# Optimization experiments

Measured on AMD Instinct MI355X. Metric: run time of the kernel, lower is better.

## Reference

```python
import jax, jax.numpy as jnp
import numpy as np

N, E, D, H, L = 50000, 400000, 128, 256, 2
ZR = 0.8          # z_ratio
GN_EPS = 1e-5     # PyG GraphNorm eps


def _graph_norm(x, w, b, a):
    # PyG GraphNorm on a single graph: x - mean_scale*mean, rms-normalize
    mu = jnp.mean(x, axis=0, keepdims=True)
    xc = x - a * mu
    var = jnp.mean(xc * xc, axis=0, keepdims=True)
    return w * xc / jnp.sqrt(var + GN_EPS) + b


def _gat(x, src, dst, W, a_src, a_dst, bias):
    # PyG GATConv, heads=1, add_self_loops=True, negative_slope=0.2.
    # edge_dim is None -> edge_attr is ignored by the layer.
    n = x.shape[0]
    loop = jnp.arange(n)
    s = jnp.concatenate([src, loop])   # [E+N]
    d = jnp.concatenate([dst, loop])
    xw = x @ W.T                        # [N,H]
    logit = jax.nn.leaky_relu((xw @ a_src)[s] + (xw @ a_dst)[d], 0.2)
    m = jax.ops.segment_max(logit, d, num_segments=n)
    ex = jnp.exp(logit - m[d])
    den = jax.ops.segment_sum(ex, d, num_segments=n)
    alpha = ex / (den[d] + 1e-16)
    return jax.ops.segment_sum(alpha[:, None] * xw[s], d, num_segments=n) + bias


def _mix(x0, x1, mask):
    return jnp.where(mask, ZR * x1 + (1.0 - ZR) * x0, ZR * x0 + (1.0 - ZR) * x1)


def _forward(x_, edge_index, edge_attr, question_embeddings, subgraph_mask,
             node_in_W, node_in_b, edge_in_W, edge_in_b, q_in_W, q_in_b,
             nqm_W, nqm_b, eqm_W, eqm_b,
             t0_W, t0_b, t1_W, t1_b,
             gat_W, gat_asrc, gat_adst, gat_bias,
             cgn_w, cgn_b, cgn_a,
             c0_W, c0_b, c1_W, c1_b,
             gn_w, gn_b, gn_a, final_W, final_b):
    src, dst = edge_index[0], edge_index[1]
    mask = subgraph_mask[:, None]
    x = jax.nn.relu(x_ @ node_in_W.T + node_in_b)                 # [N,H]
    e = jax.nn.relu(edge_attr @ edge_in_W.T + edge_in_b)          # [E,H] (unused by GAT: lin_edge is None)
    q = jax.nn.relu(question_embeddings @ q_in_W.T + q_in_b)[0]   # [1,H]
    n = x.shape[0]
    for l in range(L):
        qx = jnp.broadcast_to(q, (n, H))
        xc = jax.nn.relu(jnp.concatenate([x, qx], axis=-1) @ nqm_W[l].T + nqm_b[l])
        # torch also computes e_combined = relu(edge_question_mix([e,q])) but GATConv
        # (edge_dim=None) ignores it, so it is dead code: omitted.
        x1 = jax.nn.relu(xc @ t1_W[l].T + t1_b[l])
        x0 = jax.nn.relu(xc @ t0_W[l].T + t0_b[l])
        h = _mix(x0, x1, mask)
        h = _gat(h, src, dst, gat_W[l], gat_asrc[l], gat_adst[l], gat_bias[l])
        h = _graph_norm(h, cgn_w[l], cgn_b[l], cgn_a[l])
        # dropout p=0 -> no-op
        hc = jnp.concatenate([h, xc], axis=-1)                    # [N,2H]
        x1 = hc @ c1_W[l].T + c1_b[l]
        x0 = hc @ c0_W[l].T + c0_b[l]
        x = _mix(x0, x1, mask)
        x = _graph_norm(x, gn_w[l], gn_b[l], gn_a[l])
    # masked mean/max/add pooling over subgraph nodes (single graph)
    mk = mask.astype(x.dtype)
    cnt = jnp.sum(mk)
    x_add = jnp.sum(x * mk, axis=0, keepdims=True)
    x_mean = x_add / jnp.maximum(cnt, 1.0)
    x_max = jnp.max(jnp.where(mask, x, -jnp.inf), axis=0, keepdims=True)
    pooled = jnp.concatenate([x_mean, x_max, x_add], axis=-1)     # [1,3H]
    return pooled @ final_W.T + final_b                           # [1,H]


def setup_inputs() -> dict:
    keys = jax.random.split(jax.random.key(0), 64)
    it = iter(range(64))
    def nx(shape, s=0.05):
        return jax.random.normal(keys[next(it)], shape, jnp.float32) * s
    inp = {}
    inp['x_'] = jax.random.normal(keys[next(it)], (N, D), jnp.float32)
    inp['edge_index'] = jax.random.randint(keys[next(it)], (2, E), 0, N)
    inp['edge_attr'] = jax.random.normal(keys[next(it)], (E, D), jnp.float32)
    inp['question_embeddings'] = jax.random.normal(keys[next(it)], (1, 1, D), jnp.float32)
    inp['subgraph_mask'] = jax.random.bernoulli(keys[next(it)], 0.5, (N,))
    inp['node_in_W'] = nx((H, D)); inp['node_in_b'] = nx((H,))
    inp['edge_in_W'] = nx((H, D)); inp['edge_in_b'] = nx((H,))
    inp['q_in_W'] = nx((H, D));    inp['q_in_b'] = nx((H,))
    inp['nqm_W'] = nx((L, H, 2 * H)); inp['nqm_b'] = nx((L, H))
    inp['eqm_W'] = nx((L, H, 2 * H)); inp['eqm_b'] = nx((L, H))
    inp['t0_W'] = nx((L, H, H)); inp['t0_b'] = nx((L, H))
    inp['t1_W'] = nx((L, H, H)); inp['t1_b'] = nx((L, H))
    inp['gat_W'] = nx((L, H, H)); inp['gat_asrc'] = nx((L, H))
    inp['gat_adst'] = nx((L, H)); inp['gat_bias'] = nx((L, H))
    inp['cgn_w'] = jnp.ones((L, H)); inp['cgn_b'] = jnp.zeros((L, H)); inp['cgn_a'] = jnp.ones((L, H))
    inp['c0_W'] = nx((L, H, 2 * H)); inp['c0_b'] = nx((L, H))
    inp['c1_W'] = nx((L, H, 2 * H)); inp['c1_b'] = nx((L, H))
    inp['gn_w'] = jnp.ones((L, H)); inp['gn_b'] = jnp.zeros((L, H)); inp['gn_a'] = jnp.ones((L, H))
    inp['final_W'] = nx((H, 3 * H)); inp['final_b'] = nx((H,))
    return inp


def reference(x_, edge_index, edge_attr, question_embeddings, subgraph_mask,
              node_in_W, node_in_b, edge_in_W, edge_in_b, q_in_W, q_in_b,
              nqm_W, nqm_b, eqm_W, eqm_b,
              t0_W, t0_b, t1_W, t1_b,
              gat_W, gat_asrc, gat_adst, gat_bias,
              cgn_w, cgn_b, cgn_a,
              c0_W, c0_b, c1_W, c1_b,
              gn_w, gn_b, gn_a, final_W, final_b):
    return _forward(x_, edge_index, edge_attr, question_embeddings, subgraph_mask,
                    node_in_W, node_in_b, edge_in_W, edge_in_b, q_in_W, q_in_b,
                    nqm_W, nqm_b, eqm_W, eqm_b,
                    t0_W, t0_b, t1_W, t1_b,
                    gat_W, gat_asrc, gat_adst, gat_bias,
                    cgn_w, cgn_b, cgn_a,
                    c0_W, c0_b, c1_W, c1_b,
                    gn_w, gn_b, gn_a, final_W, final_b)
```

## Files before the change

### kernel.cpp

```cpp
#include <hip/hip_runtime.h>
#include <stdint.h>

#define NNODES 50000
#define NEDGES 400000
#define MPAD   50048
#define MTILES 391
#define ZRF    0.8f
#define GNEPS  1e-5f
#define NBLK   196

typedef unsigned short u16;
typedef __bf16 bf16x8 __attribute__((ext_vector_type(8)));
typedef float  f32x4  __attribute__((ext_vector_type(4)));

#define OFF_NODEW 0
#define OFF_NQM   32768
#define OFF_TCAT  163840
#define OFF_GAT   425984
#define OFF_CCAT  557056
#define W_TOTAL   1081344

__device__ __forceinline__ float b2f(u16 u){ union{uint32_t i; float f;} x; x.i=((uint32_t)u)<<16; return x.f; }
__device__ __forceinline__ u16 f2b(float f){ union{float f; uint32_t i;} x; x.f=f; uint32_t r=x.i+0x7FFFu+((x.i>>16)&1u); return (u16)(r>>16); }
__device__ __forceinline__ float lrelu(float x){ return x>0.f? x : 0.2f*x; }
__device__ __forceinline__ void atomicMaxF(float* a, float v){
  if (v>=0.f) atomicMax((int*)a, __float_as_int(v));
  else atomicMin((unsigned int*)a, (unsigned int)__float_as_int(v));
}

__device__ __forceinline__ void gl16(const void* g, void* l){
  __builtin_amdgcn_global_load_lds((const __attribute__((address_space(1))) void*)g,
                                   (__attribute__((address_space(3))) void*)l, 16, 0, 0);
}
__device__ __forceinline__ void bar(){
  __builtin_amdgcn_sched_barrier(0);
  asm volatile("" ::: "memory");
  __builtin_amdgcn_s_barrier();
  asm volatile("" ::: "memory");
  __builtin_amdgcn_sched_barrier(0);
}

template<int DUAL,int SPLIT,int RELU,int STATS,int DOTAV>
__device__ __forceinline__ void gemm_body(const u16* __restrict__ A0, const u16* __restrict__ A1,
    int ldA, const u16* __restrict__ B, const float* __restrict__ bias,
    u16* __restrict__ out, int ldo, int NT, int K,
    const uint32_t* __restrict__ mask, float* __restrict__ sums,
    const float* __restrict__ asrc, const float* __restrict__ adst,
    float* __restrict__ avs, float* __restrict__ avd)
{
  __shared__ alignas(16) char smem[50176];
  char* sm = smem;
  float* was = (float*)(smem + 49152);
  float* val = was + 128;

  const int tid  = threadIdx.x;
  const int nwg = gridDim.x;
  const int qc = nwg >> 3, rc = nwg & 7;
  const int xcd = blockIdx.x & 7, xi = blockIdx.x >> 3;
  const int lt = (xcd < rc ? xcd * (qc + 1) : rc * (qc + 1) + (xcd - rc) * qc) + xi;
  const int bm0 = (lt / NT) * 128;
  const int bn0 = (lt % NT) * (DUAL ? 64 : 128);

  if (DUAL && tid < 128) {
    int gr = bm0 + tid;
    int mk = (gr < NNODES) ? (mask[gr] != 0) : 0;
    was[tid] = mk ? ZRF : (1.0f - ZRF);
    val[tid] = (gr < NNODES) ? 1.0f : 0.0f;
  }

  const int lane = tid & 63;
  const int wv   = tid >> 6;
  const int wm   = (wv >> 1) * 64;
  const int wn   = (wv & 1) * (DUAL ? 32 : 64);
  const int lrow = lane & 15;
  const int kg16 = (lane >> 4) * 16;
  const int swz  = ((lrow >> 1) & 3) << 4;

  const int rA  = ((wv << 6) + lane) >> 2;
  const int gsw = (((lane & 3) ^ ((rA >> 1) & 3)) << 3);
  const u16* pa  = A0 + (size_t)(bm0 + rA) * ldA + gsw;
  const u16* pa2 = pa + 64 * ldA;
  const u16* pa1  = SPLIT ? (A1 + (size_t)(bm0 + rA) * 256 + gsw) : nullptr;
  const u16* pa12 = SPLIT ? (pa1 + 64 * 256) : nullptr;
  const u16* pb0 = B + (size_t)(bn0 + rA) * K + gsw;
  const u16* pb1 = DUAL ? (B + (size_t)(256 + bn0 + rA) * K + gsw) : (pb0 + (size_t)64 * K);
  const int dA0 = wv * 1024, dA1 = 4096 + wv * 1024;
  const int dB0 = 8192 + wv * 1024, dB1 = 12288 + wv * 1024;

  const int KT = K >> 5;
  f32x4 acc[DUAL ? 2 : 1][4][DUAL ? 2 : 4] = {};

#define STAGE(off, ktv) do { \
    int ks_ = (ktv) * 32; \
    const u16 *qa_, *qa2_; \
    if (SPLIT && ks_ >= 256) { qa_ = pa1 + (ks_ - 256); qa2_ = pa12 + (ks_ - 256); } \
    else                     { qa_ = pa + ks_;           qa2_ = pa2 + ks_; } \
    char* db_ = sm + (off); \
    gl16(qa_,       db_ + dA0); \
    gl16(qa2_,      db_ + dA1); \
    gl16(pb0 + ks_, db_ + dB0); \
    gl16(pb1 + ks_, db_ + dB1); \
  } while (0)

  STAGE(0, 0);
  if (KT > 1) STAGE(16384, 1);
  int rd = 0;
  for (int kt = 0; kt < KT; ++kt) {
    if (kt + 1 < KT) { asm volatile("s_waitcnt vmcnt(4)" ::: "memory"); }
    else             { asm volatile("s_waitcnt vmcnt(0)" ::: "memory"); }
    bar();
    if (kt + 2 < KT) { int st = rd >= 1 ? rd - 1 : 2; STAGE(st * 16384, kt + 2); }
    const char* Ab = sm + rd * 16384;
    const char* Bb = Ab + 8192;
    bf16x8 af[4];
#pragma unroll
    for (int mi = 0; mi < 4; ++mi)
      af[mi] = *(const bf16x8*)(Ab + (wm + mi * 16 + lrow) * 64 + (kg16 ^ swz));
    if (DUAL) {
#pragma unroll
      for (int ni = 0; ni < 2; ++ni) {
        int ro = (wn + ni * 16 + lrow) * 64 + (kg16 ^ swz);
        bf16x8 b0 = *(const bf16x8*)(Bb + ro);
        bf16x8 b1 = *(const bf16x8*)(Bb + 4096 + ro);
#pragma unroll
        for (int mi = 0; mi < 4; ++mi) {
          acc[0][mi][ni] = __builtin_amdgcn_mfma_f32_16x16x32_bf16(af[mi], b0, acc[0][mi][ni], 0, 0, 0);
          acc[DUAL?1:0][mi][ni] = __builtin_amdgcn_mfma_f32_16x16x32_bf16(af[mi], b1, acc[DUAL?1:0][mi][ni], 0, 0, 0);
        }
      }
    } else {
#pragma unroll
      for (int ni = 0; ni < (DUAL ? 2 : 4); ++ni) {
        bf16x8 bv = *(const bf16x8*)(Bb + (wn + ni * 16 + lrow) * 64 + (kg16 ^ swz));
#pragma unroll
        for (int mi = 0; mi < 4; ++mi)
          acc[0][mi][ni] = __builtin_amdgcn_mfma_f32_16x16x32_bf16(af[mi], bv, acc[0][mi][ni], 0, 0, 0);
      }
    }
    rd = (rd + 1 == 3) ? 0 : rd + 1;
  }
#undef STAGE
  bar();

  const int rb = (lane >> 4) * 4;
  u16* ep = (u16*)smem;
  if (DUAL) {
    float sA[2] = {0, 0}, qA[2] = {0, 0};
#pragma unroll
    for (int ni = 0; ni < 2; ++ni) {
      int coll = wn + ni * 16 + lrow;
      float b1v = bias[bn0 + coll];
      float b0v = bias[256 + bn0 + coll];
#pragma unroll
      for (int mi = 0; mi < 4; ++mi) {
        int rowl = wm + mi * 16 + rb;
#pragma unroll
        for (int r = 0; r < 4; ++r) {
          float v1 = acc[0][mi][ni][r] + b1v;
          float v0 = acc[DUAL?1:0][mi][ni][r] + b0v;
          if (RELU) { v1 = fmaxf(v1, 0.f); v0 = fmaxf(v0, 0.f); }
          float wa = was[rowl + r];
          float v = wa * v1 + (1.0f - wa) * v0;
          if (STATS) { float vl = val[rowl + r]; sA[ni] += v * vl; qA[ni] += v * v * vl; }
          ep[(rowl + r) * 72 + coll] = f2b(v);
        }
      }
    }
    bar();
#pragma unroll
    for (int p = 0; p < 4; ++p) {
      int rowl = p * 32 + (tid >> 3);
      uint4 v = *(const uint4*)&ep[rowl * 72 + (tid & 7) * 8];
      *(uint4*)&out[(size_t)(bm0 + rowl) * ldo + bn0 + (tid & 7) * 8] = v;
    }
    if (STATS) {
#pragma unroll
      for (int ni = 0; ni < 2; ++ni) {
        sA[ni] += __shfl_xor(sA[ni], 16); sA[ni] += __shfl_xor(sA[ni], 32);
        qA[ni] += __shfl_xor(qA[ni], 16); qA[ni] += __shfl_xor(qA[ni], 32);
      }
      if (lane < 16) {
#pragma unroll
        for (int ni = 0; ni < 2; ++ni) {
          int gc = bn0 + wn + ni * 16 + lane;
          atomicAdd(&sums[gc], sA[ni]);
          atomicAdd(&sums[256 + gc], qA[ni]);
        }
      }
    }
  } else {
    float sp[4][4] = {}, dp[4][4] = {};
#pragma unroll
    for (int ni = 0; ni < 4; ++ni) {
      int coll = wn + ni * 16 + lrow;
      float bv = bias ? bias[bn0 + coll] : 0.f;
      float as_ = 0.f, ad_ = 0.f;
      if (DOTAV) { as_ = asrc[bn0 + coll]; ad_ = adst[bn0 + coll]; }
#pragma unroll
      for (int mi = 0; mi < 4; ++mi) {
        int rowl = wm + mi * 16 + rb;
#pragma unroll
        for (int r = 0; r < 4; ++r) {
          float v = acc[0][mi][ni][r] + bv;
          if (RELU) v = fmaxf(v, 0.f);
          if (DOTAV) { sp[mi][r] += v * as_; dp[mi][r] += v * ad_; }
          ep[(rowl + r) * 132 + coll] = f2b(v);
        }
      }
    }
    bar();
#pragma unroll
    for (int p = 0; p < 8; ++p) {
      int rowl = p * 16 + (tid >> 4);
      uint4 v = *(const uint4*)&ep[rowl * 132 + (tid & 15) * 8];
      *(uint4*)&out[(size_t)(bm0 + rowl) * ldo + bn0 + (tid & 15) * 8] = v;
    }
    if (DOTAV) {
#pragma unroll
      for (int mi = 0; mi < 4; ++mi)
#pragma unroll
        for (int r = 0; r < 4; ++r) {
          float s_ = sp[mi][r], d_ = dp[mi][r];
          s_ += __shfl_xor(s_, 1); s_ += __shfl_xor(s_, 2); s_ += __shfl_xor(s_, 4); s_ += __shfl_xor(s_, 8);
          d_ += __shfl_xor(d_, 1); d_ += __shfl_xor(d_, 2); d_ += __shfl_xor(d_, 4); d_ += __shfl_xor(d_, 8);
          if (lrow == 0) {
            int row = bm0 + wm + mi * 16 + (lane >> 4) * 4 + r;
            atomicAdd(&avs[row], s_);
            atomicAdd(&avd[row], d_);
          }
        }
    }
  }
}

__global__ __launch_bounds__(256, 3) void g_nin(const u16* __restrict__ A, const u16* __restrict__ W,
    const float* __restrict__ b, u16* __restrict__ o)
{ gemm_body<0,0,1,0,0>(A, nullptr, 128, W, b, o, 256, 2, 128, nullptr, nullptr, nullptr, nullptr, nullptr, nullptr); }

__global__ __launch_bounds__(256, 3) void g_nqm(const u16* __restrict__ A, const u16* __restrict__ W,
    const float* __restrict__ b, u16* __restrict__ o)
{ gemm_body<0,0,1,0,0>(A, nullptr, 256, W, b, o, 256, 2, 256, nullptr, nullptr, nullptr, nullptr, nullptr, nullptr); }

__global__ __launch_bounds__(256, 3) void g_gat(const u16* __restrict__ A, const u16* __restrict__ W,
    u16* __restrict__ o, const float* __restrict__ asrc, const float* __restrict__ adst,
    float* __restrict__ avs, float* __restrict__ avd)
{ gemm_body<0,0,0,0,1>(A, nullptr, 256, W, nullptr, o, 256, 2, 256, nullptr, nullptr, asrc, adst, avs, avd); }

__global__ __launch_bounds__(256, 3) void g_tcat(const u16* __restrict__ A, const u16* __restrict__ W,
    const float* __restrict__ b, u16* __restrict__ o, const uint32_t* __restrict__ mask)
{ gemm_body<1,0,1,0,0>(A, nullptr, 256, W, b, o, 256, 4, 256, mask, nullptr, nullptr, nullptr, nullptr, nullptr); }

__global__ __launch_bounds__(256, 3) void g_ccat(const u16* __restrict__ A0, const u16* __restrict__ A1,
    const u16* __restrict__ W, const float* __restrict__ b, u16* __restrict__ o,
    const uint32_t* __restrict__ mask, float* __restrict__ sums)
{ gemm_body<1,1,0,1,0>(A0, A1, 256, W, b, o, 256, 4, 512, mask, sums, nullptr, nullptr, nullptr, nullptr); }

__global__ void foldw(const u16* __restrict__ Ws, const float* __restrict__ bs,
                      const float* __restrict__ sums, const float* __restrict__ w,
                      const float* __restrict__ b, const float* __restrict__ a,
                      int K, u16* __restrict__ Wd, float* __restrict__ bd){
  __shared__ float scs[256], shs[256];
  int n = blockIdx.x, t = threadIdx.x;
  {
    const float invn = 1.0f / (float)NNODES;
    float mu  = sums[t] * invn;
    float ex2 = sums[256 + t] * invn;
    float av  = a[t];
    float var = ex2 - (2.0f*av - av*av)*mu*mu;
    float sc  = w[t] / sqrtf(var + GNEPS);
    scs[t] = sc;
    shs[t] = b[t] - sc*av*mu;
  }
  __syncthreads();
  float bacc = 0.f;
  for (int k = t; k < K; k += 256) {
    float wv = b2f(Ws[(size_t)n * K + k]);
    if (k < 256) { bacc += wv * shs[k]; wv *= scs[k]; }
    Wd[(size_t)n * K + k] = f2b(wv);
  }
  for (int d = 32; d; d >>= 1) bacc += __shfl_xor(bacc, d);
  __shared__ float red[4];
  if ((t & 63) == 0) red[t >> 6] = bacc;
  __syncthreads();
  if (t == 0) bd[n] = bs[n] + red[0] + red[1] + red[2] + red[3];
}

__global__ void zeroall(float* __restrict__ z, int ztot, float* __restrict__ pmax){
  int i = blockIdx.x * 256 + threadIdx.x;
  if (i < 256) pmax[i] = -__builtin_inff();
  for (int j = i; j < ztot; j += gridDim.x * 256) z[j] = 0.f;
}

__global__ void convw(const float* __restrict__ nodeW, const float* __restrict__ nqmW,
                      const float* __restrict__ t0W, const float* __restrict__ t1W,
                      const float* __restrict__ gatW, const float* __restrict__ c0W,
                      const float* __restrict__ c1W, u16* __restrict__ arena){
  int idx = blockIdx.x*256 + threadIdx.x;
  if (idx >= W_TOTAL) return;
  float v;
  if (idx < OFF_NQM) { v = nodeW[idx]; }
  else if (idx < OFF_TCAT){ int i = idx - OFF_NQM;  int l=i>>16; int r=(i>>8)&255; int k=i&255; v = nqmW[l*131072 + r*512 + k]; }
  else if (idx < OFF_GAT) { int i = idx - OFF_TCAT; int l=i>>17; int n=(i>>8)&511; int k=i&255;
                            const float* s = (n<256)? t1W : t0W; v = s[l*65536 + (n&255)*256 + k]; }
  else if (idx < OFF_CCAT){ int i = idx - OFF_GAT;  v = gatW[i]; }
  else                    { int i = idx - OFF_CCAT; int l=i>>18; int n=(i>>9)&511; int k=i&511;
                            const float* s = (n<256)? c1W : c0W; v = s[l*131072 + (n&255)*512 + k]; }
  arena[idx] = f2b(v);
}

__global__ void convxin(const float* __restrict__ x, u16* __restrict__ o){
  int idx = blockIdx.x*256 + threadIdx.x;
  if (idx >= MPAD*32) return;
  int n = idx >> 5; int c = (idx & 31)*4;
  float4 v = make_float4(0.f,0.f,0.f,0.f);
  if (n < NNODES) v = *(const float4*)&x[(size_t)n*128 + c];
  ushort4 r; r.x=f2b(v.x); r.y=f2b(v.y); r.z=f2b(v.z); r.w=f2b(v.w);
  *(ushort4*)&o[(size_t)n*128 + c] = r;
}

__global__ void biascat(const float* __restrict__ t1b, const float* __restrict__ t0b,
                        const float* __restrict__ c1b, const float* __restrict__ c0b,
                        float* __restrict__ tb, float* __restrict__ cb){
  int i = blockIdx.x*256 + threadIdx.x;
  if (i >= 2048) return;
  int which = i >> 10; int j = i & 1023; int l = j >> 9; int n = j & 511;
  const float* b1 = which ? c1b : t1b;
  const float* b0 = which ? c0b : t0b;
  float v = (n < 256) ? b1[l*256 + n] : b0[l*256 + n - 256];
  (which ? cb : tb)[l*512 + n] = v;
}

__global__ void qvk(const float* __restrict__ qemb, const float* __restrict__ W,
                    const float* __restrict__ b, float* __restrict__ qv){
  int h = threadIdx.x;
  float acc = b[h];
  for (int d = 0; d < 128; ++d) acc += qemb[d] * W[h*128 + d];
  qv[h] = fmaxf(acc, 0.f);
}

__global__ void qbk(const float* __restrict__ nqmW, const float* __restrict__ nqmB,
                    const float* __restrict__ qv, float* __restrict__ qb){
  int l = blockIdx.x, h = threadIdx.x;
  const float* wr = nqmW + l*131072 + h*512 + 256;
  float acc = nqmB[l*256 + h];
  for (int j = 0; j < 256; ++j) acc += wr[j] * qv[j];
  qb[l*256 + h] = acc;
}

__global__ void detmask(const unsigned char* __restrict__ mb, int* __restrict__ cnt){
  int i = blockIdx.x*256 + threadIdx.x;
  int c = (i < NNODES) ? (mb[i] != 0) : 0;
  for (int d = 32; d; d >>= 1) c += __shfl_xor(c, d);
  __shared__ int red[4];
  if ((threadIdx.x & 63) == 0) red[threadIdx.x >> 6] = c;
  __syncthreads();
  if (threadIdx.x == 0) atomicAdd(cnt, red[0] + red[1] + red[2] + red[3]);
}

__global__ void maskmat(const void* __restrict__ m, const int* __restrict__ cnt,
                        uint32_t* __restrict__ mask){
  int i = blockIdx.x*256 + threadIdx.x;
  if (i >= NNODES) return;
  int f = ((*cnt) * 8 > NNODES * 3);
  mask[i] = f ? (((const unsigned char*)m)[i] != 0) : (((const int*)m)[i] != 0);
}

__global__ void hist(const int* __restrict__ dst, int* __restrict__ count){
  int i = blockIdx.x*256 + threadIdx.x;
  if (i < NEDGES) atomicAdd(&count[dst[i]], 1);
}

__global__ void bsum(const int* __restrict__ count, int* __restrict__ bsums){
  int b = blockIdx.x, t = threadIdx.x;
  int i = b * 256 + t;
  int v = (i < NNODES) ? count[i] : 0;
  for (int d = 32; d; d >>= 1) v += __shfl_xor(v, d);
  __shared__ int red[4];
  if ((t & 63) == 0) red[t >> 6] = v;
  __syncthreads();
  if (t == 0) bsums[b] = red[0] + red[1] + red[2] + red[3];
}

__global__ void bscan(const int* __restrict__ bsums, int* __restrict__ bpre){
  int t = threadIdx.x;
  int v = (t < NBLK) ? bsums[t] : 0;
  __shared__ int tmp[256];
  tmp[t] = v;
  __syncthreads();
  for (int d = 1; d < 256; d <<= 1) {
    int add = (t >= d) ? tmp[t - d] : 0;
    __syncthreads();
    tmp[t] += add;
    __syncthreads();
  }
  if (t < NBLK) bpre[t] = tmp[t] - v;
}

__global__ void scanblk(const int* __restrict__ count, const int* __restrict__ bpre,
                        int* __restrict__ offs, int* __restrict__ cursor){
  int b = blockIdx.x, t = threadIdx.x;
  int i = b * 256 + t;
  int v = (i < NNODES) ? count[i] : 0;
  __shared__ int tmp[256];
  tmp[t] = v;
  __syncthreads();
  for (int d = 1; d < 256; d <<= 1) {
    int add = (t >= d) ? tmp[t - d] : 0;
    __syncthreads();
    tmp[t] += add;
    __syncthreads();
  }
  int excl = bpre[b] + tmp[t] - v;
  if (i < NNODES) { offs[i] = excl; cursor[i] = excl; }
  if (i == NNODES - 1) offs[NNODES] = excl + v;
}

__global__ void scatter(const int* __restrict__ src, const int* __restrict__ dst,
                        int* __restrict__ cursor, int* __restrict__ ssrc){
  int i = blockIdx.x*256 + threadIdx.x;
  if (i >= NEDGES) return;
  int p = atomicAdd(&cursor[dst[i]], 1);
  ssrc[p] = src[i];
}

__global__ void agg(const int* __restrict__ offs, const int* __restrict__ ssrc,
                    const float* __restrict__ avs, const float* __restrict__ avd,
                    const u16* __restrict__ xw, const float* __restrict__ gbias,
                    u16* __restrict__ out){
  int v = (blockIdx.x*256 + threadIdx.x) >> 6;
  int lane = threadIdx.x & 63;
  if (v >= NNODES) return;
  int o0 = offs[v], o1 = offs[v+1];
  int deg = o1 - o0;
  float ad = avd[v];
  float slog = lrelu(avs[v] + ad);
  int c = lane*4;
  ushort4 xv = *(const ushort4*)&xw[(size_t)v*256 + c];
  float a0, a1, a2, a3;
  if (deg <= 64) {
    int s = 0; float logit = -3.0e38f;
    if (lane < deg) { s = ssrc[o0 + lane]; logit = lrelu(avs[s] + ad); }
    float m = fmaxf(slog, logit);
    for (int d = 32; d; d >>= 1) m = fmaxf(m, __shfl_xor(m, d));
    float w = (lane < deg) ? __expf(logit - m) : 0.f;
    float den = w + ((lane == 0) ? __expf(slog - m) : 0.f);
    for (int d = 32; d; d >>= 1) den += __shfl_xor(den, d);
    float rden = 1.0f / (den + 1e-16f);
    w *= rden;
    float wgt = __expf(slog - m) * rden;
    a0 = wgt*b2f(xv.x); a1 = wgt*b2f(xv.y); a2 = wgt*b2f(xv.z); a3 = wgt*b2f(xv.w);
    int i = 0;
    for (; i + 8 <= deg; i += 8) {
      ushort4 q[8]; float ww[8];
#pragma unroll
      for (int j = 0; j < 8; ++j) {
        int sj = __shfl(s, i + j); ww[j] = __shfl(w, i + j);
        q[j] = *(const ushort4*)&xw[(size_t)sj*256 + c];
      }
#pragma unroll
      for (int j = 0; j < 8; ++j) {
        a0 += ww[j]*b2f(q[j].x); a1 += ww[j]*b2f(q[j].y);
        a2 += ww[j]*b2f(q[j].z); a3 += ww[j]*b2f(q[j].w);
      }
    }
    for (; i + 4 <= deg; i += 4) {
      ushort4 q[4]; float ww[4];
#pragma unroll
      for (int j = 0; j < 4; ++j) {
        int sj = __shfl(s, i + j); ww[j] = __shfl(w, i + j);
        q[j] = *(const ushort4*)&xw[(size_t)sj*256 + c];
      }
#pragma unroll
      for (int j = 0; j < 4; ++j) {
        a0 += ww[j]*b2f(q[j].x); a1 += ww[j]*b2f(q[j].y);
        a2 += ww[j]*b2f(q[j].z); a3 += ww[j]*b2f(q[j].w);
      }
    }
    for (; i < deg; ++i) {
      int si = __shfl(s, i); float wi = __shfl(w, i);
      ushort4 q = *(const ushort4*)&xw[(size_t)si*256 + c];
      a0 += wi*b2f(q.x); a1 += wi*b2f(q.y); a2 += wi*b2f(q.z); a3 += wi*b2f(q.w);
    }
  } else {
    float m = slog;
    for (int i = o0 + lane; i < o1; i += 64) m = fmaxf(m, lrelu(avs[ssrc[i]] + ad));
    for (int d = 32; d; d >>= 1) m = fmaxf(m, __shfl_xor(m, d));
    float den = (lane == 0) ? __expf(slog - m) : 0.f;
    for (int i = o0 + lane; i < o1; i += 64) den += __expf(lrelu(avs[ssrc[i]] + ad) - m);
    for (int d = 32; d; d >>= 1) den += __shfl_xor(den, d);
    float rden = 1.0f / (den + 1e-16f);
    float wgt = __expf(slog - m) * rden;
    a0 = wgt*b2f(xv.x); a1 = wgt*b2f(xv.y); a2 = wgt*b2f(xv.z); a3 = wgt*b2f(xv.w);
    for (int i = o0; i < o1; ++i) {
      int si = ssrc[i];
      float wi = __expf(lrelu(avs[si] + ad) - m) * rden;
      ushort4 q = *(const ushort4*)&xw[(size_t)si*256 + c];
      a0 += wi*b2f(q.x); a1 += wi*b2f(q.y); a2 += wi*b2f(q.z); a3 += wi*b2f(q.w);
    }
  }
  float4 bb = *(const float4*)&gbias[c];
  ushort4 r;
  r.x = f2b(a0 + bb.x); r.y = f2b(a1 + bb.y); r.z = f2b(a2 + bb.z); r.w = f2b(a3 + bb.w);
  *(ushort4*)&out[(size_t)v*256 + c] = r;
}

__global__ void colstats(const u16* __restrict__ x, float* __restrict__ sums){
  int c = threadIdx.x;
  float s = 0.f, q = 0.f;
  for (int n = blockIdx.x; n < NNODES; n += gridDim.x){
    float v = b2f(x[(size_t)n*256 + c]); s += v; q += v*v;
  }
  atomicAdd(&sums[c], s); atomicAdd(&sums[256 + c], q);
}

__global__ void pool(const u16* __restrict__ x, const uint32_t* __restrict__ mask,
                     const float* __restrict__ sums, const float* __restrict__ w,
                     const float* __restrict__ b, const float* __restrict__ a,
                     float* __restrict__ psum, float* __restrict__ pmax, int* __restrict__ pcnt){
  int c = threadIdx.x;
  const float invn = 1.0f / (float)NNODES;
  float mu  = sums[c] * invn;
  float ex2 = sums[256 + c] * invn;
  float av  = a[c];
  float var = ex2 - (2.0f*av - av*av)*mu*mu;
  float sc  = w[c] / sqrtf(var + GNEPS);
  float sh  = b[c] - sc*av*mu;
  float s = 0.f, mx = -__builtin_inff(); int cnt = 0;
  for (int n = blockIdx.x; n < NNODES; n += gridDim.x){
    if (mask[n]){
      float v = b2f(x[(size_t)n*256 + c]) * sc + sh;
      s += v; mx = fmaxf(mx, v); cnt++;
    }
  }
  atomicAdd(&psum[c], s);
  atomicMaxF(&pmax[c], mx);
  if (c == 0) atomicAdd(pcnt, cnt);
}

__global__ void finalk(const float* __restrict__ psum, const float* __restrict__ pmax,
                       const int* __restrict__ pcnt, const float* __restrict__ W,
                       const float* __restrict__ b, float* __restrict__ out){
  int o = threadIdx.x;
  float cnt = fmaxf((float)(*pcnt), 1.0f);
  float inv = 1.0f / cnt;
  const float* wr = W + o*768;
  float acc = b[o];
  for (int j = 0; j < 256; ++j) acc += (psum[j]*inv) * wr[j];
  for (int j = 0; j < 256; ++j) acc += pmax[j] * wr[256 + j];
  for (int j = 0; j < 256; ++j) acc += psum[j] * wr[512 + j];
  out[o] = acc;
}

extern "C" void kernel_launch(void* const* d_in, const int* in_sizes, int n_in,
                              void* d_out, int out_size, void* d_ws, size_t ws_size,
                              hipStream_t stream)
{
  (void)in_sizes; (void)n_in; (void)out_size; (void)ws_size;
  const float* x_    = (const float*)d_in[0];
  const int*   eidx  = (const int*)  d_in[1];
  const float* qemb  = (const float*)d_in[3];
  const void*  mraw  =               d_in[4];
  const float* nodeW = (const float*)d_in[5];
  const float* nodeB = (const float*)d_in[6];
  const float* qinW  = (const float*)d_in[9];
  const float* qinB  = (const float*)d_in[10];
  const float* nqmW  = (const float*)d_in[11];
  const float* nqmB  = (const float*)d_in[12];
  const float* t0W   = (const float*)d_in[15];
  const float* t0B   = (const float*)d_in[16];
  const float* t1W   = (const float*)d_in[17];
  const float* t1B   = (const float*)d_in[18];
  const float* gatW  = (const float*)d_in[19];
  const float* gatAs = (const float*)d_in[20];
  const float* gatAd = (const float*)d_in[21];
  const float* gatB  = (const float*)d_in[22];
  const float* cgnW  = (const float*)d_in[23];
  const float* cgnB  = (const float*)d_in[24];
  const float* cgnA  = (const float*)d_in[25];
  const float* c0W   = (const float*)d_in[26];
  const float* c0B   = (const float*)d_in[27];
  const float* c1W   = (const float*)d_in[28];
  const float* c1B   = (const float*)d_in[29];
  const float* gnW   = (const float*)d_in[30];
  const float* gnB   = (const float*)d_in[31];
  const float* gnA   = (const float*)d_in[32];
  const float* finW  = (const float*)d_in[33];
  const float* finB  = (const float*)d_in[34];
  float* outp = (float*)d_out;

  char* p = (char*)d_ws;
  auto alloc = [&](size_t b)->char*{ char* r = p; p += (b + 511) & ~(size_t)511; return r; };
  u16*      arena = (u16*)     alloc((size_t)W_TOTAL*2);
  u16*      wtc   = (u16*)     alloc((size_t)512*512*2);
  u16*      wtn   = (u16*)     alloc((size_t)256*256*2);
  float*    btc   = (float*)   alloc(512*4);
  float*    qbt   = (float*)   alloc(256*4);
  float*    tb    = (float*)   alloc(1024*4);
  float*    cb    = (float*)   alloc(1024*4);
  float*    qv    = (float*)   alloc(256*4);
  float*    qb    = (float*)   alloc(512*4);
  float*    pmax  = (float*)   alloc(256*4);
  uint32_t* mask  = (uint32_t*)alloc((size_t)NNODES*4);
  int*      offs  = (int*)     alloc((size_t)(NNODES+1)*4);
  int*      cursor= (int*)     alloc((size_t)NNODES*4);
  int*      ssrc  = (int*)     alloc((size_t)NEDGES*4);
  int*      bsums = (int*)     alloc((size_t)NBLK*4);
  int*      bpre  = (int*)     alloc((size_t)NBLK*4);

  const int Z_COUNT = 0;
  const int Z_SUMS  = 50048;
  const int Z_AV    = Z_SUMS + 2048;
  const int Z_PSUM  = Z_AV + 4*MPAD;
  const int Z_PCNT  = Z_PSUM + 256;
  const int Z_MCNT  = Z_PCNT + 64;
  const int ZTOT    = Z_MCNT + 64;
  float*    zar   = (float*)   alloc((size_t)ZTOT*4);
  int*      count = (int*)(zar + Z_COUNT);
  float*    sumsC0= zar + Z_SUMS;
  float*    sumsC1= zar + Z_SUMS + 512;
  float*    sumsG0= zar + Z_SUMS + 1024;
  float*    sumsG1= zar + Z_SUMS + 1536;
  float*    av    = zar + Z_AV;
  float*    psum  = zar + Z_PSUM;
  int*      pcnt  = (int*)(zar + Z_PCNT);
  int*      mcnt  = (int*)(zar + Z_MCNT);

  u16*      xin   = (u16*)     alloc((size_t)MPAD*128*2);
  u16*      xb    = (u16*)     alloc((size_t)MPAD*256*2);
  u16*      xc    = (u16*)     alloc((size_t)MPAD*256*2);
  u16*      hb    = (u16*)     alloc((size_t)MPAD*256*2);
  u16*      xw    = (u16*)     alloc((size_t)MPAD*256*2);
  u16*      hgat  = (u16*)     alloc((size_t)MPAD*256*2);
  u16*      xm    = (u16*)     alloc((size_t)MPAD*256*2);

  const int* esrc = eidx;
  const int* edst = eidx + NEDGES;

  zeroall<<<dim3(256), dim3(256), 0, stream>>>(zar, ZTOT, pmax);
  convw  <<<dim3((W_TOTAL+255)/256), dim3(256), 0, stream>>>(nodeW, nqmW, t0W, t1W, gatW, c0W, c1W, arena);
  convxin<<<dim3(MPAD*32/256), dim3(256), 0, stream>>>(x_, xin);
  biascat<<<dim3(8), dim3(256), 0, stream>>>(t1B, t0B, c1B, c0B, tb, cb);
  qvk    <<<dim3(1), dim3(256), 0, stream>>>(qemb, qinW, qinB, qv);
  qbk    <<<dim3(2), dim3(256), 0, stream>>>(nqmW, nqmB, qv, qb);
  detmask<<<dim3(NBLK), dim3(256), 0, stream>>>((const unsigned char*)mraw, mcnt);
  maskmat<<<dim3((NNODES+255)/256), dim3(256), 0, stream>>>(mraw, mcnt, mask);
  hist   <<<dim3((NEDGES+255)/256), dim3(256), 0, stream>>>(edst, count);
  bsum   <<<dim3(NBLK), dim3(256), 0, stream>>>(count, bsums);
  bscan  <<<dim3(1), dim3(256), 0, stream>>>(bsums, bpre);
  scanblk<<<dim3(NBLK), dim3(256), 0, stream>>>(count, bpre, offs, cursor);
  scatter<<<dim3((NEDGES+255)/256), dim3(256), 0, stream>>>(esrc, edst, cursor, ssrc);

  g_nin<<<dim3(MTILES*2), dim3(256), 0, stream>>>(xin, arena+OFF_NODEW, nodeB, xb);

  for (int l = 0; l < 2; ++l) {
    float* avs_l = av + l*2*MPAD;
    float* avd_l = avs_l + MPAD;
    float* sumsC = l ? sumsC1 : sumsC0;
    float* sumsG = l ? sumsG1 : sumsG0;
    if (l == 0)
      g_nqm<<<dim3(MTILES*2), dim3(256), 0, stream>>>(xb, arena+OFF_NQM, qb, xc);
    else
      g_nqm<<<dim3(MTILES*2), dim3(256), 0, stream>>>(xm, wtn, qbt, xc);
    g_tcat<<<dim3(MTILES*4), dim3(256), 0, stream>>>(xc, arena+OFF_TCAT + l*131072, tb + l*512, hb, mask);
    g_gat<<<dim3(MTILES*2), dim3(256), 0, stream>>>(hb, arena+OFF_GAT + l*65536, xw,
                                                    gatAs + l*256, gatAd + l*256, avs_l, avd_l);
    agg  <<<dim3(12500), dim3(256), 0, stream>>>(offs, ssrc, avs_l, avd_l, xw, gatB + l*256, hgat);
    colstats<<<dim3(1024), dim3(256), 0, stream>>>(hgat, sumsC);
    foldw   <<<dim3(512), dim3(256), 0, stream>>>(arena+OFF_CCAT + l*262144, cb + l*512,
                                                  sumsC, cgnW + l*256, cgnB + l*256, cgnA + l*256, 512, wtc, btc);
    g_ccat<<<dim3(MTILES*4), dim3(256), 0, stream>>>(hgat, xc, wtc, btc, xm, mask, sumsG);
    if (l == 0)
      foldw<<<dim3(256), dim3(256), 0, stream>>>(arena+OFF_NQM + 65536, qb + 256,
                                                 sumsG, gnW, gnB, gnA, 256, wtn, qbt);
  }

  pool  <<<dim3(512), dim3(256), 0, stream>>>(xm, mask, sumsG1, gnW + 256, gnB + 256, gnA + 256, psum, pmax, pcnt);
  finalk<<<dim3(1), dim3(256), 0, stream>>>(psum, pmax, pcnt, finW, finB, outp);
}
```

Measured before the change: 537.7 us.

## Fuse node-question mix, transform mix and GAT projection into one kernel

Replaces three separate GEMM launches (nqm, tcat, gat) per layer with a single kernel. Each 64-row tile keeps its intermediate activations in LDS and streams the weight chunks through shared memory. This removes the global round trips for the hb intermediate and the atomics for the attention dot products, which are now written directly. It also merges the two small question kernels into one. The trade-off is a smaller M tile (64 rows), lower occupancy (launch bounds 2) and serialized weight staging with full waits, which could reduce MFMA efficiency.

```diff
diff --git a/kernel.cpp b/kernel.cpp
--- a/kernel.cpp
+++ b/kernel.cpp
@@ -40,13 +40,189 @@
   __builtin_amdgcn_sched_barrier(0);
 }
 
-template<int DUAL,int SPLIT,int RELU,int STATS,int DOTAV>
+__global__ __launch_bounds__(256, 2) void fuse3(
+    const u16* __restrict__ X, const u16* __restrict__ Wn, const float* __restrict__ qb_,
+    const u16* __restrict__ Wt, const float* __restrict__ bt,
+    const u16* __restrict__ Wg,
+    const float* __restrict__ asrc, const float* __restrict__ adst,
+    const uint32_t* __restrict__ mask,
+    u16* __restrict__ xc, u16* __restrict__ xw,
+    float* __restrict__ avs, float* __restrict__ avd)
+{
+  __shared__ alignas(16) u16 bufA[16384];
+  __shared__ alignas(16) u16 bufC[16384];
+  __shared__ float wam[64];
+
+  const int tid  = threadIdx.x;
+  const int lane = tid & 63, wv = tid >> 6;
+  const int lrow = lane & 15;
+  const int kq   = lane >> 4;
+
+  const int nwg = gridDim.x;
+  const int qc = nwg >> 3, rc = nwg & 7;
+  const int xcd = blockIdx.x & 7, xi = blockIdx.x >> 3;
+  const int lt = (xcd < rc ? xcd*(qc+1) : rc*(qc+1) + (xcd-rc)*qc) + xi;
+  const int bm0 = lt * 64;
+
+  const int sr  = tid >> 2;
+  const int sgp = tid & 3;
+  const int ssw = (sr >> 1) & 3;
+  const int rloc = (wv << 4) + lrow;
+  const int asw  = (rloc >> 1) & 3;
+
+#define LDSB(buf, kt, r, q) ((char*)(buf) + (kt)*4096 + (r)*64 + (((q) ^ (((r)>>1)&3))<<4))
+#define BFRAG(kt, br) (*(const bf16x8*)LDSB(bufA, kt, br, kq))
+
+#pragma unroll
+  for (int kt = 0; kt < 8; ++kt)
+    gl16(X + (size_t)(bm0 + sr)*256 + kt*32 + ((sgp ^ ssw)<<3),
+         (char*)bufA + kt*4096 + tid*16);
+  { int gr = bm0 + rloc;
+    wam[rloc] = (gr < NNODES && mask[gr]) ? ZRF : (1.0f - ZRF); }
+  asm volatile("s_waitcnt vmcnt(0)" ::: "memory");
+  bf16x8 af[8];
+#pragma unroll
+  for (int kt = 0; kt < 8; ++kt)
+    af[kt] = *(const bf16x8*)LDSB(bufA, kt, rloc, kq);
+  bar();
+
+#define STAGEB(Wp, rowexpr) do { _Pragma("unroll") for (int kt = 0; kt < 8; ++kt) { \
+    int br_ = (rowexpr); \
+    gl16((Wp) + (size_t)br_*256 + kt*32 + ((sgp ^ ssw)<<3), (char*)bufA + kt*4096 + tid*16); } } while (0)
+
+#define WFRAG(col, v0_, v1_, v2_, v3_) do { \
+    int kt_ = (col) >> 5, cc_ = (col) & 31, g_ = cc_ >> 3, pos_ = cc_ & 7; \
+    float vv_[4] = { v0_, v1_, v2_, v3_ }; \
+    _Pragma("unroll") for (int r_ = 0; r_ < 4; ++r_) { \
+      int rd_ = (wv<<4) + (kq<<2) + r_; \
+      *(u16*)(LDSB(bufC, kt_, rd_, g_) + pos_*2) = f2b(vv_[r_]); } } while (0)
+
+  STAGEB(Wn, 64*0 + sr);
+  for (int c = 0; c < 4; ++c) {
+    asm volatile("s_waitcnt vmcnt(0)" ::: "memory");
+    bar();
+    f32x4 a0 = {}, a1 = {}, a2 = {}, a3 = {};
+#pragma unroll
+    for (int kt = 0; kt < 8; ++kt) {
+      bf16x8 b0 = BFRAG(kt, 0*16 + lrow), b1 = BFRAG(kt, 1*16 + lrow);
+      bf16x8 b2 = BFRAG(kt, 2*16 + lrow), b3 = BFRAG(kt, 3*16 + lrow);
+      a0 = __builtin_amdgcn_mfma_f32_16x16x32_bf16(af[kt], b0, a0, 0, 0, 0);
+      a1 = __builtin_amdgcn_mfma_f32_16x16x32_bf16(af[kt], b1, a1, 0, 0, 0);
+      a2 = __builtin_amdgcn_mfma_f32_16x16x32_bf16(af[kt], b2, a2, 0, 0, 0);
+      a3 = __builtin_amdgcn_mfma_f32_16x16x32_bf16(af[kt], b3, a3, 0, 0, 0);
+    }
+    bar();
+    if (c + 1 < 4) STAGEB(Wn, 64*(c+1) + sr);
+#pragma unroll
+    for (int nf = 0; nf < 4; ++nf) {
+      int col = c*64 + nf*16 + lrow;
+      float bb = qb_[col];
+      f32x4 aa = (nf==0)?a0:(nf==1)?a1:(nf==2)?a2:a3;
+      WFRAG(col, fmaxf(aa[0]+bb,0.f), fmaxf(aa[1]+bb,0.f), fmaxf(aa[2]+bb,0.f), fmaxf(aa[3]+bb,0.f));
+    }
+  }
+
+#pragma unroll
+  for (int kt = 0; kt < 8; ++kt)
+    af[kt] = *(const bf16x8*)LDSB(bufC, kt, rloc, kq);
+#pragma unroll
+  for (int kt = 0; kt < 8; ++kt) {
+    uint4 v = *(const uint4*)LDSB(bufC, kt, sr, sgp);
+    *(uint4*)&xc[(size_t)(bm0 + sr)*256 + kt*32 + sgp*8] = v;
+  }
+
+  STAGEB(Wt, (sr < 32) ? (32*0 + sr) : (256 + 32*0 + (sr - 32)));
+  for (int c = 0; c < 8; ++c) {
+    asm volatile("s_waitcnt vmcnt(0)" ::: "memory");
+    bar();
+    f32x4 p10 = {}, p11 = {}, p00 = {}, p01 = {};
+#pragma unroll
+    for (int kt = 0; kt < 8; ++kt) {
+      bf16x8 b10 = BFRAG(kt, 0*16 + lrow), b11 = BFRAG(kt, 1*16 + lrow);
+      bf16x8 b00 = BFRAG(kt, 32 + 0*16 + lrow), b01 = BFRAG(kt, 32 + 1*16 + lrow);
+      p10 = __builtin_amdgcn_mfma_f32_16x16x32_bf16(af[kt], b10, p10, 0, 0, 0);
+      p11 = __builtin_amdgcn_mfma_f32_16x16x32_bf16(af[kt], b11, p11, 0, 0, 0);
+      p00 = __builtin_amdgcn_mfma_f32_16x16x32_bf16(af[kt], b00, p00, 0, 0, 0);
+      p01 = __builtin_amdgcn_mfma_f32_16x16x32_bf16(af[kt], b01, p01, 0, 0, 0);
+    }
+    bar();
+    if (c + 1 < 8) STAGEB(Wt, (sr < 32) ? (32*(c+1) + sr) : (256 + 32*(c+1) + (sr - 32)));
+#pragma unroll
+    for (int nf = 0; nf < 2; ++nf) {
+      int col = c*32 + nf*16 + lrow;
+      float b1v = bt[col], b0v = bt[256 + col];
+      f32x4 v1 = nf ? p11 : p10;
+      f32x4 v0 = nf ? p01 : p00;
+      int kt_ = col >> 5, cc_ = col & 31, g_ = cc_ >> 3, pos_ = cc_ & 7;
+#pragma unroll
+      for (int r_ = 0; r_ < 4; ++r_) {
+        int rd_ = (wv<<4) + (kq<<2) + r_;
+        float wa = wam[rd_];
+        float hv = wa * fmaxf(v1[r_] + b1v, 0.f) + (1.0f - wa) * fmaxf(v0[r_] + b0v, 0.f);
+        *(u16*)(LDSB(bufC, kt_, rd_, g_) + pos_*2) = f2b(hv);
+      }
+    }
+  }
+
+#pragma unroll
+  for (int kt = 0; kt < 8; ++kt)
+    af[kt] = *(const bf16x8*)LDSB(bufC, kt, rloc, kq);
+
+  float sp[4] = {0,0,0,0}, dp[4] = {0,0,0,0};
+  STAGEB(Wg, 64*0 + sr);
+  for (int c = 0; c < 4; ++c) {
+    asm volatile("s_waitcnt vmcnt(0)" ::: "memory");
+    bar();
+    f32x4 a0 = {}, a1 = {}, a2 = {}, a3 = {};
+#pragma unroll
+    for (int kt = 0; kt < 8; ++kt) {
+      bf16x8 b0 = BFRAG(kt, 0*16 + lrow), b1 = BFRAG(kt, 1*16 + lrow);
+      bf16x8 b2 = BFRAG(kt, 2*16 + lrow), b3 = BFRAG(kt, 3*16 + lrow);
+      a0 = __builtin_amdgcn_mfma_f32_16x16x32_bf16(af[kt], b0, a0, 0, 0, 0);
+      a1 = __builtin_amdgcn_mfma_f32_16x16x32_bf16(af[kt], b1, a1, 0, 0, 0);
+      a2 = __builtin_amdgcn_mfma_f32_16x16x32_bf16(af[kt], b2, a2, 0, 0, 0);
+      a3 = __builtin_amdgcn_mfma_f32_16x16x32_bf16(af[kt], b3, a3, 0, 0, 0);
+    }
+    bar();
+    if (c + 1 < 4) STAGEB(Wg, 64*(c+1) + sr);
+#pragma unroll
+    for (int nf = 0; nf < 4; ++nf) {
+      int col = c*64 + nf*16 + lrow;
+      float as_ = asrc[col], ad_ = adst[col];
+      f32x4 aa = (nf==0)?a0:(nf==1)?a1:(nf==2)?a2:a3;
+#pragma unroll
+      for (int r_ = 0; r_ < 4; ++r_) { sp[r_] += aa[r_]*as_; dp[r_] += aa[r_]*ad_; }
+      WFRAG(col, aa[0], aa[1], aa[2], aa[3]);
+    }
+  }
+
+#pragma unroll
+  for (int r_ = 0; r_ < 4; ++r_) {
+    float s_ = sp[r_], d_ = dp[r_];
+    s_ += __shfl_xor(s_, 1); s_ += __shfl_xor(s_, 2); s_ += __shfl_xor(s_, 4); s_ += __shfl_xor(s_, 8);
+    d_ += __shfl_xor(d_, 1); d_ += __shfl_xor(d_, 2); d_ += __shfl_xor(d_, 4); d_ += __shfl_xor(d_, 8);
+    if (lrow == 0) {
+      int row = bm0 + (wv<<4) + (kq<<2) + r_;
+      avs[row] = s_;
+      avd[row] = d_;
+    }
+  }
+#pragma unroll
+  for (int kt = 0; kt < 8; ++kt) {
+    uint4 v = *(const uint4*)LDSB(bufC, kt, sr, sgp);
+    *(uint4*)&xw[(size_t)(bm0 + sr)*256 + kt*32 + sgp*8] = v;
+  }
+#undef LDSB
+#undef BFRAG
+#undef STAGEB
+#undef WFRAG
+}
+
+template<int DUAL,int SPLIT,int RELU,int STATS>
 __device__ __forceinline__ void gemm_body(const u16* __restrict__ A0, const u16* __restrict__ A1,
     int ldA, const u16* __restrict__ B, const float* __restrict__ bias,
     u16* __restrict__ out, int ldo, int NT, int K,
-    const uint32_t* __restrict__ mask, float* __restrict__ sums,
-    const float* __restrict__ asrc, const float* __restrict__ adst,
-    float* __restrict__ avs, float* __restrict__ avd)
+    const uint32_t* __restrict__ mask, float* __restrict__ sums)
 {
   __shared__ alignas(16) char smem[50176];
   char* sm = smem;
@@ -189,13 +365,10 @@
       }
     }
   } else {
-    float sp[4][4] = {}, dp[4][4] = {};
 #pragma unroll
     for (int ni = 0; ni < 4; ++ni) {
       int coll = wn + ni * 16 + lrow;
       float bv = bias ? bias[bn0 + coll] : 0.f;
-      float as_ = 0.f, ad_ = 0.f;
-      if (DOTAV) { as_ = asrc[bn0 + coll]; ad_ = adst[bn0 + coll]; }
 #pragma unroll
       for (int mi = 0; mi < 4; ++mi) {
         int rowl = wm + mi * 16 + rb;
@@ -203,7 +376,6 @@
         for (int r = 0; r < 4; ++r) {
           float v = acc[0][mi][ni][r] + bv;
           if (RELU) v = fmaxf(v, 0.f);
-          if (DOTAV) { sp[mi][r] += v * as_; dp[mi][r] += v * ad_; }
           ep[(rowl + r) * 132 + coll] = f2b(v);
         }
       }
@@ -215,45 +387,17 @@
       uint4 v = *(const uint4*)&ep[rowl * 132 + (tid & 15) * 8];
       *(uint4*)&out[(size_t)(bm0 + rowl) * ldo + bn0 + (tid & 15) * 8] = v;
     }
-    if (DOTAV) {
-#pragma unroll
-      for (int mi = 0; mi < 4; ++mi)
-#pragma unroll
-        for (int r = 0; r < 4; ++r) {
-          float s_ = sp[mi][r], d_ = dp[mi][r];
-          s_ += __shfl_xor(s_, 1); s_ += __shfl_xor(s_, 2); s_ += __shfl_xor(s_, 4); s_ += __shfl_xor(s_, 8);
-          d_ += __shfl_xor(d_, 1); d_ += __shfl_xor(d_, 2); d_ += __shfl_xor(d_, 4); d_ += __shfl_xor(d_, 8);
-          if (lrow == 0) {
-            int row = bm0 + wm + mi * 16 + (lane >> 4) * 4 + r;
-            atomicAdd(&avs[row], s_);
-            atomicAdd(&avd[row], d_);
-          }
-        }
-    }
   }
 }
 
 __global__ __launch_bounds__(256, 3) void g_nin(const u16* __restrict__ A, const u16* __restrict__ W,
     const float* __restrict__ b, u16* __restrict__ o)
-{ gemm_body<0,0,1,0,0>(A, nullptr, 128, W, b, o, 256, 2, 128, nullptr, nullptr, nullptr, nullptr, nullptr, nullptr); }
-
-__global__ __launch_bounds__(256, 3) void g_nqm(const u16* __restrict__ A, const u16* __restrict__ W,
-    const float* __restrict__ b, u16* __restrict__ o)
-{ gemm_body<0,0,1,0,0>(A, nullptr, 256, W, b, o, 256, 2, 256, nullptr, nullptr, nullptr, nullptr, nullptr, nullptr); }
-
-__global__ __launch_bounds__(256, 3) void g_gat(const u16* __restrict__ A, const u16* __restrict__ W,
-    u16* __restrict__ o, const float* __restrict__ asrc, const float* __restrict__ adst,
-    float* __restrict__ avs, float* __restrict__ avd)
-{ gemm_body<0,0,0,0,1>(A, nullptr, 256, W, nullptr, o, 256, 2, 256, nullptr, nullptr, asrc, adst, avs, avd); }
-
-__global__ __launch_bounds__(256, 3) void g_tcat(const u16* __restrict__ A, const u16* __restrict__ W,
-    const float* __restrict__ b, u16* __restrict__ o, const uint32_t* __restrict__ mask)
-{ gemm_body<1,0,1,0,0>(A, nullptr, 256, W, b, o, 256, 4, 256, mask, nullptr, nullptr, nullptr, nullptr, nullptr); }
+{ gemm_body<0,0,1,0>(A, nullptr, 128, W, b, o, 256, 2, 128, nullptr, nullptr); }
 
 __global__ __launch_bounds__(256, 3) void g_ccat(const u16* __restrict__ A0, const u16* __restrict__ A1,
     const u16* __restrict__ W, const float* __restrict__ b, u16* __restrict__ o,
     const uint32_t* __restrict__ mask, float* __restrict__ sums)
-{ gemm_body<1,1,0,1,0>(A0, A1, 256, W, b, o, 256, 4, 512, mask, sums, nullptr, nullptr, nullptr, nullptr); }
+{ gemm_body<1,1,0,1>(A0, A1, 256, W, b, o, 256, 4, 512, mask, sums); }
 
 __global__ void foldw(const u16* __restrict__ Ws, const float* __restrict__ bs,
                       const float* __restrict__ sums, const float* __restrict__ w,
@@ -330,21 +474,21 @@
   (which ? cb : tb)[l*512 + n] = v;
 }
 
-__global__ void qvk(const float* __restrict__ qemb, const float* __restrict__ W,
-                    const float* __restrict__ b, float* __restrict__ qv){
+__global__ void qk(const float* __restrict__ qemb, const float* __restrict__ qinW,
+                   const float* __restrict__ qinB, const float* __restrict__ nqmW,
+                   const float* __restrict__ nqmB, float* __restrict__ qb){
+  __shared__ float qvs[256];
   int h = threadIdx.x;
-  float acc = b[h];
-  for (int d = 0; d < 128; ++d) acc += qemb[d] * W[h*128 + d];
-  qv[h] = fmaxf(acc, 0.f);
-}
-
-__global__ void qbk(const float* __restrict__ nqmW, const float* __restrict__ nqmB,
-                    const float* __restrict__ qv, float* __restrict__ qb){
-  int l = blockIdx.x, h = threadIdx.x;
-  const float* wr = nqmW + l*131072 + h*512 + 256;
-  float acc = nqmB[l*256 + h];
-  for (int j = 0; j < 256; ++j) acc += wr[j] * qv[j];
-  qb[l*256 + h] = acc;
+  float a = qinB[h];
+  for (int d = 0; d < 128; ++d) a += qemb[d] * qinW[h*128 + d];
+  qvs[h] = fmaxf(a, 0.f);
+  __syncthreads();
+  for (int l = 0; l < 2; ++l) {
+    const float* wr = nqmW + l*131072 + h*512 + 256;
+    float acc = nqmB[l*256 + h];
+    for (int j = 0; j < 256; ++j) acc += wr[j] * qvs[j];
+    qb[l*256 + h] = acc;
+  }
 }
 
 __global__ void detmask(const unsigned char* __restrict__ mb, int* __restrict__ cnt){
@@ -597,7 +741,6 @@
   float*    qbt   = (float*)   alloc(256*4);
   float*    tb    = (float*)   alloc(1024*4);
   float*    cb    = (float*)   alloc(1024*4);
-  float*    qv    = (float*)   alloc(256*4);
   float*    qb    = (float*)   alloc(512*4);
   float*    pmax  = (float*)   alloc(256*4);
   uint32_t* mask  = (uint32_t*)alloc((size_t)NNODES*4);
@@ -607,7 +750,6 @@
   int*      bsums = (int*)     alloc((size_t)NBLK*4);
   int*      bpre  = (int*)     alloc((size_t)NBLK*4);
 
-  const int Z_COUNT = 0;
   const int Z_SUMS  = 50048;
   const int Z_AV    = Z_SUMS + 2048;
   const int Z_PSUM  = Z_AV + 4*MPAD;
@@ -615,7 +757,7 @@
   const int Z_MCNT  = Z_PCNT + 64;
   const int ZTOT    = Z_MCNT + 64;
   float*    zar   = (float*)   alloc((size_t)ZTOT*4);
-  int*      count = (int*)(zar + Z_COUNT);
+  int*      count = (int*)zar;
   float*    sumsC0= zar + Z_SUMS;
   float*    sumsC1= zar + Z_SUMS + 512;
   float*    sumsG0= zar + Z_SUMS + 1024;
@@ -628,7 +770,6 @@
   u16*      xin   = (u16*)     alloc((size_t)MPAD*128*2);
   u16*      xb    = (u16*)     alloc((size_t)MPAD*256*2);
   u16*      xc    = (u16*)     alloc((size_t)MPAD*256*2);
-  u16*      hb    = (u16*)     alloc((size_t)MPAD*256*2);
   u16*      xw    = (u16*)     alloc((size_t)MPAD*256*2);
   u16*      hgat  = (u16*)     alloc((size_t)MPAD*256*2);
   u16*      xm    = (u16*)     alloc((size_t)MPAD*256*2);
@@ -640,8 +781,7 @@
   convw  <<<dim3((W_TOTAL+255)/256), dim3(256), 0, stream>>>(nodeW, nqmW, t0W, t1W, gatW, c0W, c1W, arena);
   convxin<<<dim3(MPAD*32/256), dim3(256), 0, stream>>>(x_, xin);
   biascat<<<dim3(8), dim3(256), 0, stream>>>(t1B, t0B, c1B, c0B, tb, cb);
-  qvk    <<<dim3(1), dim3(256), 0, stream>>>(qemb, qinW, qinB, qv);
-  qbk    <<<dim3(2), dim3(256), 0, stream>>>(nqmW, nqmB, qv, qb);
+  qk     <<<dim3(1), dim3(256), 0, stream>>>(qemb, qinW, qinB, nqmW, nqmB, qb);
   detmask<<<dim3(NBLK), dim3(256), 0, stream>>>((const unsigned char*)mraw, mcnt);
   maskmat<<<dim3((NNODES+255)/256), dim3(256), 0, stream>>>(mraw, mcnt, mask);
   hist   <<<dim3((NEDGES+255)/256), dim3(256), 0, stream>>>(edst, count);
@@ -657,14 +797,12 @@
     float* avd_l = avs_l + MPAD;
     float* sumsC = l ? sumsC1 : sumsC0;
     float* sumsG = l ? sumsG1 : sumsG0;
-    if (l == 0)
-      g_nqm<<<dim3(MTILES*2), dim3(256), 0, stream>>>(xb, arena+OFF_NQM, qb, xc);
-    else
-      g_nqm<<<dim3(MTILES*2), dim3(256), 0, stream>>>(xm, wtn, qbt, xc);
-    g_tcat<<<dim3(MTILES*4), dim3(256), 0, stream>>>(xc, arena+OFF_TCAT + l*131072, tb + l*512, hb, mask);
-    g_gat<<<dim3(MTILES*2), dim3(256), 0, stream>>>(hb, arena+OFF_GAT + l*65536, xw,
-                                                    gatAs + l*256, gatAd + l*256, avs_l, avd_l);
-    agg  <<<dim3(12500), dim3(256), 0, stream>>>(offs, ssrc, avs_l, avd_l, xw, gatB + l*256, hgat);
+    fuse3<<<dim3(MPAD/64), dim3(256), 0, stream>>>(
+        l ? xm : xb, l ? wtn : (arena+OFF_NQM), l ? qbt : qb,
+        arena+OFF_TCAT + l*131072, tb + l*512,
+        arena+OFF_GAT + l*65536,
+        gatAs + l*256, gatAd + l*256, mask, xc, xw, avs_l, avd_l);
+    agg<<<dim3(12500), dim3(256), 0, stream>>>(offs, ssrc, avs_l, avd_l, xw, gatB + l*256, hgat);
     colstats<<<dim3(1024), dim3(256), 0, stream>>>(hgat, sumsC);
     foldw   <<<dim3(512), dim3(256), 0, stream>>>(arena+OFF_CCAT + l*262144, cb + l*512,
                                                   sumsC, cgnW + l*256, cgnB + l*256, cgnA + l*256, 512, wtc, btc);
```

Result: no change. 534.5 us (-0.6%).
